# Kernel optimization log

Hardware: AMD Instinct MI355X
Metric: run time of the kernel (lower is better)

The kernel has to match this reference:

```python
import jax, jax.numpy as jnp
import numpy as np

N = 50000      # num nodes
E = 800000     # num edges
IN = 512       # in_feats (= num_hidden)
H = 8          # num_heads
D = 64         # out_feats per head (H*D = 512)
NEG_SLOPE = 0.2


def setup_inputs() -> dict:
    key = jax.random.key(0)
    ks = jax.random.split(key, 7)
    feat = jax.random.normal(ks[0], (N, IN), jnp.float32)
    src = jax.random.randint(ks[1], (E,), 0, N)
    dst = jax.random.randint(ks[2], (E,), 0, N)
    W_fc = jax.random.normal(ks[3], (IN, H * D), jnp.float32) * (1.0 / np.sqrt(IN))
    W_res = jax.random.normal(ks[4], (IN, H * D), jnp.float32) * (1.0 / np.sqrt(IN))
    attn_l = jax.random.normal(ks[5], (1, H, D), jnp.float32) * 0.1
    attn_r = jax.random.normal(ks[6], (1, H, D), jnp.float32) * 0.1
    return {"feat": feat, "src": src, "dst": dst, "W_fc": W_fc,
            "W_res": W_res, "attn_l": attn_l, "attn_r": attn_r}


def reference(feat, src, dst, W_fc, W_res, attn_l, attn_r):
    # fc: [N, IN] @ [IN, H*D] -> [N, H, D]
    ft = (feat @ W_fc).reshape(N, H, D)
    # attention logits per node: el = sum(ft * attn_l, -1), er likewise -> [N, H]
    el = jnp.sum(ft * attn_l, axis=-1)
    er = jnp.sum(ft * attn_r, axis=-1)
    # u_add_v on edges, then LeakyReLU -> [E, H]
    e = jax.nn.leaky_relu(el[src] + er[dst], negative_slope=NEG_SLOPE)
    # edge_softmax: normalize over incoming edges of each dst node
    m = jax.ops.segment_max(e, dst, num_segments=N)            # [N, H]
    m = jnp.where(jnp.isfinite(m), m, jnp.zeros_like(m))       # guard zero-in-degree
    ex = jnp.exp(e - m[dst])                                   # [E, H]
    s = jax.ops.segment_sum(ex, dst, num_segments=N)           # [N, H]
    a = ex / jnp.maximum(s[dst], 1e-9)                         # [E, H]
    # u_mul_e + sum aggregation: gather src features, weight, scatter-add to dst
    msg = ft[src] * a[:, :, None]                              # [E, H, D]
    rst = jax.ops.segment_sum(msg, dst, num_segments=N)        # [N, H, D]
    # residual: res_fc Linear since in_dst_feats != out_feats
    rst = rst + (feat @ W_res).reshape(N, H, D)
    return rst
```

## Files before the change

### kernel.cpp

```cpp
#include <hip/hip_runtime.h>
#include <hip/hip_bf16.h>

#define NN 50000
#define EE 800000
#define INF 512
#define HH 8
#define DD 64
#define HD 512

typedef unsigned short u16;
typedef u16 u16x4 __attribute__((ext_vector_type(4)));
typedef u16 u16x8 __attribute__((ext_vector_type(8)));
typedef __bf16 bf16x8 __attribute__((ext_vector_type(8)));
typedef float f32x4 __attribute__((ext_vector_type(4)));

__device__ __forceinline__ float bf2f(u16 u) {
    return __uint_as_float(((unsigned)u) << 16);
}
__device__ __forceinline__ u16 f2bf(float f) {
    __hip_bfloat16 h = __float2bfloat16(f);
    return *reinterpret_cast<u16*>(&h);
}

__device__ __forceinline__ void gload_lds16(const void* g, void* l) {
    __builtin_amdgcn_global_load_lds(
        (const __attribute__((address_space(1))) void*)g,
        (__attribute__((address_space(3))) void*)l, 16, 0, 0);
}

__global__ __launch_bounds__(256) void sniff5_kernel(const u16* __restrict__ p0,
                                                     const u16* __restrict__ p1,
                                                     const u16* __restrict__ p2,
                                                     const u16* __restrict__ p3,
                                                     const u16* __restrict__ p4,
                                                     int* __restrict__ flags) {
    const u16* ps[5] = {p0, p1, p2, p3, p4};
    const u16* p = ps[blockIdx.x];
    __shared__ int bad;
    if (threadIdx.x == 0) bad = 0;
    __syncthreads();
    float v = fabsf(bf2f(p[2 * threadIdx.x]));
    if (!(v < 1e4f)) atomicAdd(&bad, 1);
    __syncthreads();
    if (threadIdx.x == 0) flags[blockIdx.x] = (bad >= 8) ? 1 : 0;
}

__global__ __launch_bounds__(256) void convert_kernel(const void* __restrict__ in,
                                                      u16* __restrict__ out,
                                                      const int* __restrict__ flag) {
    const int isf32 = *flag;
    const int total = NN * INF / 8;
    for (int i = blockIdx.x * 256 + threadIdx.x; i < total; i += gridDim.x * 256) {
        if (isf32) {
            f32x4 a = ((const f32x4*)in)[2 * i];
            f32x4 b = ((const f32x4*)in)[2 * i + 1];
            u16x8 w;
#pragma unroll
            for (int j = 0; j < 4; ++j) { w[j] = f2bf(a[j]); w[4 + j] = f2bf(b[j]); }
            ((u16x8*)out)[i] = w;
        } else {
            ((u16x8*)out)[i] = ((const u16x8*)in)[i];
        }
    }
}

__global__ __launch_bounds__(256) void transpose_kernel(const void* __restrict__ in,
                                                        u16* __restrict__ out,
                                                        const int* __restrict__ flag) {
    __shared__ u16 tile[64][65];
    const int isf32 = *flag;
    int tr = (blockIdx.x & 7) * 64;
    int tc = (blockIdx.x >> 3) * 64;
    for (int idx = threadIdx.x; idx < 64 * 64; idx += 256) {
        int r = idx >> 6, c = idx & 63;
        int g = (tr + r) * 512 + tc + c;
        tile[r][c] = isf32 ? f2bf(((const float*)in)[g]) : ((const u16*)in)[g];
    }
    __syncthreads();
    for (int idx = threadIdx.x; idx < 64 * 64; idx += 256) {
        int r = idx >> 6, c = idx & 63;
        out[(tc + r) * 512 + tr + c] = tile[c][r];
    }
}

__global__ void zero_deg_kernel(int* __restrict__ deg) {
    int t = blockIdx.x * 256 + threadIdx.x;
    if (t < NN) deg[t] = 0;
}

__global__ void count_kernel(const int* __restrict__ dst, int* __restrict__ deg) {
    int e = blockIdx.x * 256 + threadIdx.x;
    if (e < EE) atomicAdd(&deg[dst[e]], 1);
}

#define SCAN_CH 49
__global__ __launch_bounds__(1024) void scan_kernel(const int* __restrict__ deg,
                                                    int* __restrict__ rowptr,
                                                    int* __restrict__ cursor) {
    __shared__ int sums[1024];
    int t = threadIdx.x;
    int base = t * SCAN_CH;
    int s = 0;
    for (int k = 0; k < SCAN_CH; ++k) {
        int i = base + k;
        if (i < NN) s += deg[i];
    }
    sums[t] = s;
    __syncthreads();
    for (int off = 1; off < 1024; off <<= 1) {
        int v = (t >= off) ? sums[t - off] : 0;
        __syncthreads();
        sums[t] += v;
        __syncthreads();
    }
    int run = (t == 0) ? 0 : sums[t - 1];
    for (int k = 0; k < SCAN_CH; ++k) {
        int i = base + k;
        if (i < NN) {
            rowptr[i] = run;
            cursor[i] = run;
            run += deg[i];
        }
    }
    if (t == 0) rowptr[NN] = EE;
}

__global__ void scatter_kernel(const int* __restrict__ src, const int* __restrict__ dst,
                               int* __restrict__ cursor, int* __restrict__ csr_src) {
    int e = blockIdx.x * 256 + threadIdx.x;
    if (e < EE) {
        int p = atomicAdd(&cursor[dst[e]], 1);
        csr_src[p] = src[e];
    }
}

#define TM 128
#define TN 128
#define BK 64
#define NT (INF / BK)
#define NMBLK 392

__global__ __launch_bounds__(256, 5) void gemm_kernel(const u16* __restrict__ Ab,
                                                      const u16* __restrict__ Wt,
                                                      u16* __restrict__ ft,
                                                      float* __restrict__ outf) {
    __shared__ u16 Asm[TM * BK];
    __shared__ u16 Bsm[TN * BK];

    const int bid = blockIdx.x;
    const int r8 = bid & 7;
    const int q = bid >> 3;
    const int m0 = (((q >> 3) << 3) | r8) * TM;
    const int n0 = (q & 7) * TN;
    const int tid = threadIdx.x;
    const int lane = tid & 63;
    const int wave = tid >> 6;
    const int wr = (wave >> 1) * 64;
    const int wc = (wave & 1) * 64;
    const int lrow = lane & 15;
    const int quad = lane >> 4;

    const int rg = lane >> 3;
    const int ch = lane & 7;
    const int cs = ch ^ rg;

    const u16* asrc[4];
    const u16* bsrc[4];
    u16* adst[4];
    u16* bdst[4];
#pragma unroll
    for (int g = 0; g < 4; ++g) {
        int G = wave * 4 + g;
        int r = G * 8 + rg;
        int gr = m0 + r; gr = gr < NN ? gr : NN - 1;
        asrc[g] = Ab + (size_t)gr * INF + cs * 8;
        bsrc[g] = Wt + (size_t)(n0 + r) * INF + cs * 8;
        adst[g] = Asm + G * 512;
        bdst[g] = Bsm + G * 512;
    }

    f32x4 acc[4][4] = {};

    for (int t = 0; t < NT; ++t) {
        const int k0 = t * BK;
        __syncthreads();
#pragma unroll
        for (int g = 0; g < 4; ++g) {
            gload_lds16(asrc[g] + k0, adst[g]);
            gload_lds16(bsrc[g] + k0, bdst[g]);
        }
        __syncthreads();

#pragma unroll
        for (int ks = 0; ks < 2; ++ks) {
            bf16x8 af[4], bfr[4];
#pragma unroll
            for (int mi = 0; mi < 4; ++mi) {
                int ar = wr + mi * 16 + lrow;
                int sc = (ks * 4 + quad) ^ (ar & 7);
                u16x8 tv = *(const u16x8*)(Asm + ar * 64 + sc * 8);
                af[mi] = *(bf16x8*)&tv;
            }
#pragma unroll
            for (int ni = 0; ni < 4; ++ni) {
                int br = wc + ni * 16 + lrow;
                int sc = (ks * 4 + quad) ^ (br & 7);
                u16x8 tv = *(const u16x8*)(Bsm + br * 64 + sc * 8);
                bfr[ni] = *(bf16x8*)&tv;
            }
#pragma unroll
            for (int mi = 0; mi < 4; ++mi)
#pragma unroll
                for (int ni = 0; ni < 4; ++ni)
                    acc[mi][ni] = __builtin_amdgcn_mfma_f32_16x16x32_bf16(af[mi], bfr[ni],
                                                                          acc[mi][ni], 0, 0, 0);
        }
    }

#pragma unroll
    for (int mi = 0; mi < 4; ++mi) {
        int rb = m0 + wr + mi * 16 + quad * 4;
#pragma unroll
        for (int ni = 0; ni < 4; ++ni) {
            int col = n0 + wc + ni * 16 + lrow;
#pragma unroll
            for (int r = 0; r < 4; ++r) {
                int row = rb + r;
                if (row < NN) {
                    float v = acc[mi][ni][r];
                    if (col < HD) ft[row * HD + col] = f2bf(v);
                    else outf[row * HD + (col - HD)] = v;
                }
            }
        }
    }
}

__global__ __launch_bounds__(256) void attn_dot_kernel(const u16* __restrict__ ft,
                                                       const void* __restrict__ al,
                                                       const void* __restrict__ ar,
                                                       float* __restrict__ el,
                                                       float* __restrict__ er,
                                                       const int* __restrict__ flags) {
    int node = blockIdx.x * 4 + (threadIdx.x >> 6);
    if (node >= NN) return;
    int lane = threadIdx.x & 63;
    int off = lane * 8;

    float wl[8], wr_[8];
    if (flags[3]) {
        f32x4 a0 = *(const f32x4*)((const float*)al + off);
        f32x4 a1 = *(const f32x4*)((const float*)al + off + 4);
#pragma unroll
        for (int j = 0; j < 4; ++j) { wl[j] = a0[j]; wl[4 + j] = a1[j]; }
    } else {
        u16x8 a = *(const u16x8*)((const u16*)al + off);
#pragma unroll
        for (int j = 0; j < 8; ++j) wl[j] = bf2f(a[j]);
    }
    if (flags[4]) {
        f32x4 a0 = *(const f32x4*)((const float*)ar + off);
        f32x4 a1 = *(const f32x4*)((const float*)ar + off + 4);
#pragma unroll
        for (int j = 0; j < 4; ++j) { wr_[j] = a0[j]; wr_[4 + j] = a1[j]; }
    } else {
        u16x8 a = *(const u16x8*)((const u16*)ar + off);
#pragma unroll
        for (int j = 0; j < 8; ++j) wr_[j] = bf2f(a[j]);
    }

    u16x8 f = *(const u16x8*)(ft + node * HD + off);
    float vl = 0.0f, vr = 0.0f;
#pragma unroll
    for (int j = 0; j < 8; ++j) {
        float x = bf2f(f[j]);
        vl += x * wl[j];
        vr += x * wr_[j];
    }
#pragma unroll
    for (int msk = 1; msk < 8; msk <<= 1) {
        vl += __shfl_xor(vl, msk);
        vr += __shfl_xor(vr, msk);
    }
    if ((lane & 7) == 0) {
        el[node * HH + (lane >> 3)] = vl;
        er[node * HH + (lane >> 3)] = vr;
    }
}

__global__ __launch_bounds__(256) void aggregate_kernel(const int* __restrict__ rowptr,
                                                        const int* __restrict__ csr_src,
                                                        const u16* __restrict__ ft,
                                                        const float* __restrict__ el,
                                                        const float* __restrict__ er,
                                                        float* __restrict__ outf) {
    int node = blockIdx.x * 2 + (threadIdx.x >> 7);
    if (node >= NN) return;
    int half = (threadIdx.x >> 6) & 1;
    int lane = threadIdx.x & 63;
    int ebase = half * 256 + lane * 4;
    int head = ebase >> 6;
    int beg = rowptr[node], end = rowptr[node + 1];
    float erd = er[node * HH + head];

    float sden = 0.0f;
    float acc0 = 0.f, acc1 = 0.f, acc2 = 0.f, acc3 = 0.f;

    if (beg < end) {
        const int last = end - 1;
        float elp0, elp1, elp2, elp3;
        u16x4 fp0, fp1, fp2, fp3;
        int sn0, sn1, sn2, sn3;
        {
            int c0 = csr_src[min(beg + 0, last)];
            int c1 = csr_src[min(beg + 1, last)];
            int c2 = csr_src[min(beg + 2, last)];
            int c3 = csr_src[min(beg + 3, last)];
            elp0 = el[c0 * HH + head]; fp0 = *(const u16x4*)(ft + c0 * HD + ebase);
            elp1 = el[c1 * HH + head]; fp1 = *(const u16x4*)(ft + c1 * HD + ebase);
            elp2 = el[c2 * HH + head]; fp2 = *(const u16x4*)(ft + c2 * HD + ebase);
            elp3 = el[c3 * HH + head]; fp3 = *(const u16x4*)(ft + c3 * HD + ebase);
            sn0 = csr_src[min(beg + 4, last)];
            sn1 = csr_src[min(beg + 5, last)];
            sn2 = csr_src[min(beg + 6, last)];
            sn3 = csr_src[min(beg + 7, last)];
        }
        for (int base = beg; base < end; base += 4) {
#define PROC(K)                                                              \
            {                                                                \
                float elv = elp##K;                                          \
                u16x4 f = fp##K;                                             \
                int s = sn##K;                                               \
                elp##K = el[s * HH + head];                                  \
                fp##K = *(const u16x4*)(ft + s * HD + ebase);                \
                sn##K = csr_src[min(base + 8 + K, last)];                    \
                float v = elv + erd;                                         \
                v = v > 0.0f ? v : 0.2f * v;                                 \
                v = fminf(v, 75.0f);                                         \
                float ex = __expf(v);                                        \
                ex = (base + K < end) ? ex : 0.0f;                           \
                sden += ex;                                                  \
                acc0 += bf2f(f[0]) * ex;                                     \
                acc1 += bf2f(f[1]) * ex;                                     \
                acc2 += bf2f(f[2]) * ex;                                     \
                acc3 += bf2f(f[3]) * ex;                                     \
            }
            PROC(0) PROC(1) PROC(2) PROC(3)
#undef PROC
        }
    }

    float inv = 1.0f / fmaxf(sden, 1e-9f);
    float* op = outf + node * HD + ebase;
    f32x4 r = *(const f32x4*)op;
    f32x4 o;
    o[0] = acc0 * inv + r[0];
    o[1] = acc1 * inv + r[1];
    o[2] = acc2 * inv + r[2];
    o[3] = acc3 * inv + r[3];
    *(f32x4*)op = o;
}

extern "C" void kernel_launch(void* const* d_in, const int* in_sizes, int n_in,
                              void* d_out, int out_size, void* d_ws, size_t ws_size,
                              hipStream_t stream) {
    const void* feat   = d_in[0];
    const int*  src    = (const int*)d_in[1];
    const int*  dst    = (const int*)d_in[2];
    const void* W_fc   = d_in[3];
    const void* W_res  = d_in[4];
    const void* attn_l = d_in[5];
    const void* attn_r = d_in[6];
    float* outf = (float*)d_out;

    char* ws = (char*)d_ws;
    int*   flags   = (int*)(ws);
    u16*   Wt      = (u16*)(ws + 256);
    u16*   ft      = (u16*)(ws + 1048832);
    float* el      = (float*)(ws + 52248832);
    float* er      = (float*)(ws + 53848832);
    int*   deg     = (int*)(ws + 55448832);
    int*   rowptr  = (int*)(ws + 55648832);
    int*   cursor  = (int*)(ws + 55848896);
    int*   csr_src = (int*)(ws + 56048896);
    u16*   feat16  = (u16*)(ws + 59248896);

    sniff5_kernel<<<5, 256, 0, stream>>>((const u16*)feat, (const u16*)W_fc,
                                         (const u16*)W_res, (const u16*)attn_l,
                                         (const u16*)attn_r, flags);
    convert_kernel<<<2048, 256, 0, stream>>>(feat, feat16, flags + 0);
    transpose_kernel<<<64, 256, 0, stream>>>(W_fc, Wt, flags + 1);
    transpose_kernel<<<64, 256, 0, stream>>>(W_res, Wt + 512 * 512, flags + 2);

    zero_deg_kernel<<<(NN + 255) / 256, 256, 0, stream>>>(deg);
    count_kernel<<<(EE + 255) / 256, 256, 0, stream>>>(dst, deg);
    scan_kernel<<<1, 1024, 0, stream>>>(deg, rowptr, cursor);
    scatter_kernel<<<(EE + 255) / 256, 256, 0, stream>>>(src, dst, cursor, csr_src);

    gemm_kernel<<<NMBLK * 8, 256, 0, stream>>>(feat16, Wt, ft, outf);

    attn_dot_kernel<<<(NN + 3) / 4, 256, 0, stream>>>(ft, attn_l, attn_r, el, er, flags);
    aggregate_kernel<<<(NN + 1) / 2, 256, 0, stream>>>(rowptr, csr_src, ft, el, er, outf);
}
```

Measured before the change: 670.2 us.

## Precompute per-edge attention weights in a separate kernel before aggregation

Adds an edge_weight_kernel that computes exp(leaky_relu(el[src]+er[dst])) for every CSR edge and head, and stores the results contiguously in CSR order. The aggregation kernel then streams these weights instead of gathering el[src] and computing the exponential inline. This turns one random gather per edge into a sequential read. The cost is an extra kernel launch, a 25.6MB weight buffer written and read back, and a csr_dst array written during scatter. The ew buffer reuses the feat16 workspace region, which is safe only because the GEMM has already consumed feat16 by then.

```diff
diff --git a/kernel.cpp b/kernel.cpp
--- a/kernel.cpp
+++ b/kernel.cpp
@@ -126,11 +126,14 @@
 }
 
 __global__ void scatter_kernel(const int* __restrict__ src, const int* __restrict__ dst,
-                               int* __restrict__ cursor, int* __restrict__ csr_src) {
+                               int* __restrict__ cursor, int* __restrict__ csr_src,
+                               int* __restrict__ csr_dst) {
     int e = blockIdx.x * 256 + threadIdx.x;
     if (e < EE) {
-        int p = atomicAdd(&cursor[dst[e]], 1);
+        int d = dst[e];
+        int p = atomicAdd(&cursor[d], 1);
         csr_src[p] = src[e];
+        csr_dst[p] = d;
     }
 }
 
@@ -288,11 +291,27 @@
     }
 }
 
+__global__ __launch_bounds__(256) void edge_weight_kernel(const int* __restrict__ csr_src,
+                                                          const int* __restrict__ csr_dst,
+                                                          const float* __restrict__ el,
+                                                          const float* __restrict__ er,
+                                                          float* __restrict__ ew) {
+    int t = blockIdx.x * 256 + threadIdx.x;
+    int p = t >> 3;
+    if (p >= EE) return;
+    int h = t & 7;
+    int s = csr_src[p];
+    int d = csr_dst[p];
+    float v = el[s * HH + h] + er[d * HH + h];
+    v = v > 0.0f ? v : 0.2f * v;
+    v = fminf(v, 75.0f);
+    ew[p * HH + h] = __expf(v);
+}
+
 __global__ __launch_bounds__(256) void aggregate_kernel(const int* __restrict__ rowptr,
                                                         const int* __restrict__ csr_src,
+                                                        const float* __restrict__ ew,
                                                         const u16* __restrict__ ft,
-                                                        const float* __restrict__ el,
-                                                        const float* __restrict__ er,
                                                         float* __restrict__ outf) {
     int node = blockIdx.x * 2 + (threadIdx.x >> 7);
     if (node >= NN) return;
@@ -301,14 +320,13 @@
     int ebase = half * 256 + lane * 4;
     int head = ebase >> 6;
     int beg = rowptr[node], end = rowptr[node + 1];
-    float erd = er[node * HH + head];
 
     float sden = 0.0f;
     float acc0 = 0.f, acc1 = 0.f, acc2 = 0.f, acc3 = 0.f;
 
     if (beg < end) {
         const int last = end - 1;
-        float elp0, elp1, elp2, elp3;
+        float wp0, wp1, wp2, wp3;
         u16x4 fp0, fp1, fp2, fp3;
         int sn0, sn1, sn2, sn3;
         {
@@ -316,10 +334,14 @@
             int c1 = csr_src[min(beg + 1, last)];
             int c2 = csr_src[min(beg + 2, last)];
             int c3 = csr_src[min(beg + 3, last)];
-            elp0 = el[c0 * HH + head]; fp0 = *(const u16x4*)(ft + c0 * HD + ebase);
-            elp1 = el[c1 * HH + head]; fp1 = *(const u16x4*)(ft + c1 * HD + ebase);
-            elp2 = el[c2 * HH + head]; fp2 = *(const u16x4*)(ft + c2 * HD + ebase);
-            elp3 = el[c3 * HH + head]; fp3 = *(const u16x4*)(ft + c3 * HD + ebase);
+            wp0 = ew[min(beg + 0, last) * HH + head];
+            wp1 = ew[min(beg + 1, last) * HH + head];
+            wp2 = ew[min(beg + 2, last) * HH + head];
+            wp3 = ew[min(beg + 3, last) * HH + head];
+            fp0 = *(const u16x4*)(ft + c0 * HD + ebase);
+            fp1 = *(const u16x4*)(ft + c1 * HD + ebase);
+            fp2 = *(const u16x4*)(ft + c2 * HD + ebase);
+            fp3 = *(const u16x4*)(ft + c3 * HD + ebase);
             sn0 = csr_src[min(beg + 4, last)];
             sn1 = csr_src[min(beg + 5, last)];
             sn2 = csr_src[min(beg + 6, last)];
@@ -328,22 +350,17 @@
         for (int base = beg; base < end; base += 4) {
 #define PROC(K)                                                              \
             {                                                                \
-                float elv = elp##K;                                          \
+                float w = (base + K < end) ? wp##K : 0.0f;                   \
                 u16x4 f = fp##K;                                             \
                 int s = sn##K;                                               \
-                elp##K = el[s * HH + head];                                  \
+                wp##K = ew[min(base + 4 + K, last) * HH + head];             \
                 fp##K = *(const u16x4*)(ft + s * HD + ebase);                \
                 sn##K = csr_src[min(base + 8 + K, last)];                    \
-                float v = elv + erd;                                         \
-                v = v > 0.0f ? v : 0.2f * v;                                 \
-                v = fminf(v, 75.0f);                                         \
-                float ex = __expf(v);                                        \
-                ex = (base + K < end) ? ex : 0.0f;                           \
-                sden += ex;                                                  \
-                acc0 += bf2f(f[0]) * ex;                                     \
-                acc1 += bf2f(f[1]) * ex;                                     \
-                acc2 += bf2f(f[2]) * ex;                                     \
-                acc3 += bf2f(f[3]) * ex;                                     \
+                sden += w;                                                   \
+                acc0 += bf2f(f[0]) * w;                                      \
+                acc1 += bf2f(f[1]) * w;                                      \
+                acc2 += bf2f(f[2]) * w;                                      \
+                acc3 += bf2f(f[3]) * w;                                      \
             }
             PROC(0) PROC(1) PROC(2) PROC(3)
 #undef PROC
@@ -384,6 +401,8 @@
     int*   cursor  = (int*)(ws + 55848896);
     int*   csr_src = (int*)(ws + 56048896);
     u16*   feat16  = (u16*)(ws + 59248896);
+    float* ew      = (float*)(ws + 59248896);
+    int*   csr_dst = (int*)(ws + 110448896);
 
     sniff5_kernel<<<5, 256, 0, stream>>>((const u16*)feat, (const u16*)W_fc,
                                          (const u16*)W_res, (const u16*)attn_l,
@@ -395,10 +414,11 @@
     zero_deg_kernel<<<(NN + 255) / 256, 256, 0, stream>>>(deg);
     count_kernel<<<(EE + 255) / 256, 256, 0, stream>>>(dst, deg);
     scan_kernel<<<1, 1024, 0, stream>>>(deg, rowptr, cursor);
-    scatter_kernel<<<(EE + 255) / 256, 256, 0, stream>>>(src, dst, cursor, csr_src);
+    scatter_kernel<<<(EE + 255) / 256, 256, 0, stream>>>(src, dst, cursor, csr_src, csr_dst);
 
     gemm_kernel<<<NMBLK * 8, 256, 0, stream>>>(feat16, Wt, ft, outf);
 
     attn_dot_kernel<<<(NN + 3) / 4, 256, 0, stream>>>(ft, attn_l, attn_r, el, er, flags);
-    aggregate_kernel<<<(NN + 1) / 2, 256, 0, stream>>>(rowptr, csr_src, ft, el, er, outf);
-}
+    edge_weight_kernel<<<EE * 8 / 256, 256, 0, stream>>>(csr_src, csr_dst, el, er, ew);
+    aggregate_kernel<<<(NN + 1) / 2, 256, 0, stream>>>(rowptr, csr_src, ew, ft, outf);
+}
```

After: 690.1 us. 1.03x slower.

## Fuse prep kernels into one launch and compute attention dots in GEMM epilogue

Applied to the files above, without the earlier changes.

Merges the dtype sniff, feature conversion, weight transposes and degree zeroing into a single prep kernel in which each block sniffs its own input. The el/er attention dot products are now computed from the fp32 GEMM accumulators in the epilogue, using shuffles across the 16 lanes, so the separate attn_dot pass that re-read ft is gone. This saves several launches and one full read of the bf16 ft array. In exchange every conversion block repeats the sniff, and the GEMM epilogue gains extra shuffles and possible register pressure. el/er also now come from fp32 accumulators rather than rounded bf16, which changes numerics slightly.

```diff
diff --git a/kernel.cpp b/kernel.cpp
--- a/kernel.cpp
+++ b/kernel.cpp
@@ -28,64 +28,68 @@
         (__attribute__((address_space(3))) void*)l, 16, 0, 0);
 }
 
-__global__ __launch_bounds__(256) void sniff5_kernel(const u16* __restrict__ p0,
-                                                     const u16* __restrict__ p1,
-                                                     const u16* __restrict__ p2,
-                                                     const u16* __restrict__ p3,
-                                                     const u16* __restrict__ p4,
-                                                     int* __restrict__ flags) {
-    const u16* ps[5] = {p0, p1, p2, p3, p4};
-    const u16* p = ps[blockIdx.x];
-    __shared__ int bad;
-    if (threadIdx.x == 0) bad = 0;
+__device__ __forceinline__ int sniff_region(const u16* __restrict__ p, int* vote) {
+    int tid = threadIdx.x;
+    if (tid == 0) *vote = 0;
     __syncthreads();
-    float v = fabsf(bf2f(p[2 * threadIdx.x]));
-    if (!(v < 1e4f)) atomicAdd(&bad, 1);
+    float v = fabsf(bf2f(p[2 * tid]));
+    if (!(v < 1e4f)) atomicAdd(vote, 1);
     __syncthreads();
-    if (threadIdx.x == 0) flags[blockIdx.x] = (bad >= 8) ? 1 : 0;
-}
-
-__global__ __launch_bounds__(256) void convert_kernel(const void* __restrict__ in,
-                                                      u16* __restrict__ out,
-                                                      const int* __restrict__ flag) {
-    const int isf32 = *flag;
-    const int total = NN * INF / 8;
-    for (int i = blockIdx.x * 256 + threadIdx.x; i < total; i += gridDim.x * 256) {
-        if (isf32) {
-            f32x4 a = ((const f32x4*)in)[2 * i];
-            f32x4 b = ((const f32x4*)in)[2 * i + 1];
-            u16x8 w;
-#pragma unroll
-            for (int j = 0; j < 4; ++j) { w[j] = f2bf(a[j]); w[4 + j] = f2bf(b[j]); }
-            ((u16x8*)out)[i] = w;
-        } else {
-            ((u16x8*)out)[i] = ((const u16x8*)in)[i];
-        }
-    }
-}
-
-__global__ __launch_bounds__(256) void transpose_kernel(const void* __restrict__ in,
-                                                        u16* __restrict__ out,
-                                                        const int* __restrict__ flag) {
+    int r = (*vote >= 8) ? 1 : 0;
+    __syncthreads();
+    return r;
+}
+
+#define PREP_CONV 2048
+#define PREP_TR   (PREP_CONV + 128)
+#define PREP_ZERO (PREP_TR + 196)
+
+__global__ __launch_bounds__(256) void prep_kernel(const void* __restrict__ feat,
+                                                   u16* __restrict__ feat16,
+                                                   const void* __restrict__ W_fc,
+                                                   const void* __restrict__ W_res,
+                                                   u16* __restrict__ Wt,
+                                                   int* __restrict__ deg) {
     __shared__ u16 tile[64][65];
-    const int isf32 = *flag;
-    int tr = (blockIdx.x & 7) * 64;
-    int tc = (blockIdx.x >> 3) * 64;
-    for (int idx = threadIdx.x; idx < 64 * 64; idx += 256) {
-        int r = idx >> 6, c = idx & 63;
-        int g = (tr + r) * 512 + tc + c;
-        tile[r][c] = isf32 ? f2bf(((const float*)in)[g]) : ((const u16*)in)[g];
-    }
-    __syncthreads();
-    for (int idx = threadIdx.x; idx < 64 * 64; idx += 256) {
-        int r = idx >> 6, c = idx & 63;
-        out[(tc + r) * 512 + tr + c] = tile[c][r];
-    }
-}
-
-__global__ void zero_deg_kernel(int* __restrict__ deg) {
-    int t = blockIdx.x * 256 + threadIdx.x;
-    if (t < NN) deg[t] = 0;
+    const int bid = blockIdx.x;
+    const int tid = threadIdx.x;
+    if (bid < PREP_CONV) {
+        const int isf32 = sniff_region((const u16*)feat, (int*)&tile[0][0]);
+        const int total = NN * INF / 8;
+        for (int i = bid * 256 + tid; i < total; i += PREP_CONV * 256) {
+            if (isf32) {
+                f32x4 a = ((const f32x4*)feat)[2 * i];
+                f32x4 b = ((const f32x4*)feat)[2 * i + 1];
+                u16x8 w;
+#pragma unroll
+                for (int j = 0; j < 4; ++j) { w[j] = f2bf(a[j]); w[4 + j] = f2bf(b[j]); }
+                ((u16x8*)feat16)[i] = w;
+            } else {
+                ((u16x8*)feat16)[i] = ((const u16x8*)feat)[i];
+            }
+        }
+    } else if (bid < PREP_TR) {
+        const int w = bid - PREP_CONV;
+        const void* in = (w < 64) ? W_fc : W_res;
+        u16* out = Wt + ((w < 64) ? 0 : 512 * 512);
+        const int tb = w & 63;
+        const int isf32 = sniff_region((const u16*)in, (int*)&tile[0][0]);
+        int tr = (tb & 7) * 64;
+        int tc = (tb >> 3) * 64;
+        for (int idx = tid; idx < 64 * 64; idx += 256) {
+            int r = idx >> 6, c = idx & 63;
+            int g = (tr + r) * 512 + tc + c;
+            tile[r][c] = isf32 ? f2bf(((const float*)in)[g]) : ((const u16*)in)[g];
+        }
+        __syncthreads();
+        for (int idx = tid; idx < 64 * 64; idx += 256) {
+            int r = idx >> 6, c = idx & 63;
+            out[(tc + r) * 512 + tr + c] = tile[c][r];
+        }
+    } else {
+        int t = (bid - PREP_TR) * 256 + tid;
+        if (t < NN) deg[t] = 0;
+    }
 }
 
 __global__ void count_kernel(const int* __restrict__ dst, int* __restrict__ deg) {
@@ -143,7 +147,11 @@
 __global__ __launch_bounds__(256, 5) void gemm_kernel(const u16* __restrict__ Ab,
                                                       const u16* __restrict__ Wt,
                                                       u16* __restrict__ ft,
-                                                      float* __restrict__ outf) {
+                                                      float* __restrict__ outf,
+                                                      const void* __restrict__ al,
+                                                      const void* __restrict__ ar,
+                                                      float* __restrict__ el,
+                                                      float* __restrict__ er) {
     __shared__ u16 Asm[TM * BK];
     __shared__ u16 Bsm[TN * BK];
 
@@ -196,9 +204,9 @@
             bf16x8 af[4], bfr[4];
 #pragma unroll
             for (int mi = 0; mi < 4; ++mi) {
-                int ar = wr + mi * 16 + lrow;
-                int sc = (ks * 4 + quad) ^ (ar & 7);
-                u16x8 tv = *(const u16x8*)(Asm + ar * 64 + sc * 8);
+                int ar_ = wr + mi * 16 + lrow;
+                int sc = (ks * 4 + quad) ^ (ar_ & 7);
+                u16x8 tv = *(const u16x8*)(Asm + ar_ * 64 + sc * 8);
                 af[mi] = *(bf16x8*)&tv;
             }
 #pragma unroll
@@ -234,57 +242,41 @@
             }
         }
     }
-}
-
-__global__ __launch_bounds__(256) void attn_dot_kernel(const u16* __restrict__ ft,
-                                                       const void* __restrict__ al,
-                                                       const void* __restrict__ ar,
-                                                       float* __restrict__ el,
-                                                       float* __restrict__ er,
-                                                       const int* __restrict__ flags) {
-    int node = blockIdx.x * 4 + (threadIdx.x >> 6);
-    if (node >= NN) return;
-    int lane = threadIdx.x & 63;
-    int off = lane * 8;
-
-    float wl[8], wr_[8];
-    if (flags[3]) {
-        f32x4 a0 = *(const f32x4*)((const float*)al + off);
-        f32x4 a1 = *(const f32x4*)((const float*)al + off + 4);
-#pragma unroll
-        for (int j = 0; j < 4; ++j) { wl[j] = a0[j]; wl[4 + j] = a1[j]; }
-    } else {
-        u16x8 a = *(const u16x8*)((const u16*)al + off);
-#pragma unroll
-        for (int j = 0; j < 8; ++j) wl[j] = bf2f(a[j]);
-    }
-    if (flags[4]) {
-        f32x4 a0 = *(const f32x4*)((const float*)ar + off);
-        f32x4 a1 = *(const f32x4*)((const float*)ar + off + 4);
-#pragma unroll
-        for (int j = 0; j < 4; ++j) { wr_[j] = a0[j]; wr_[4 + j] = a1[j]; }
-    } else {
-        u16x8 a = *(const u16x8*)((const u16*)ar + off);
-#pragma unroll
-        for (int j = 0; j < 8; ++j) wr_[j] = bf2f(a[j]);
-    }
-
-    u16x8 f = *(const u16x8*)(ft + node * HD + off);
-    float vl = 0.0f, vr = 0.0f;
-#pragma unroll
-    for (int j = 0; j < 8; ++j) {
-        float x = bf2f(f[j]);
-        vl += x * wl[j];
-        vr += x * wr_[j];
-    }
-#pragma unroll
-    for (int msk = 1; msk < 8; msk <<= 1) {
-        vl += __shfl_xor(vl, msk);
-        vr += __shfl_xor(vr, msk);
-    }
-    if ((lane & 7) == 0) {
-        el[node * HH + (lane >> 3)] = vl;
-        er[node * HH + (lane >> 3)] = vr;
+
+    if (n0 < HD) {
+        __syncthreads();
+        const int fal = sniff_region((const u16*)al, (int*)Asm);
+        const int far_ = sniff_region((const u16*)ar, (int*)Asm);
+        const int h = (n0 >> 6) + (wc >> 6);
+        float alv[4], arv[4];
+#pragma unroll
+        for (int ni = 0; ni < 4; ++ni) {
+            int idx = h * DD + ni * 16 + lrow;
+            alv[ni] = fal ? ((const float*)al)[idx] : bf2f(((const u16*)al)[idx]);
+            arv[ni] = far_ ? ((const float*)ar)[idx] : bf2f(((const u16*)ar)[idx]);
+        }
+#pragma unroll
+        for (int mi = 0; mi < 4; ++mi) {
+#pragma unroll
+            for (int r = 0; r < 4; ++r) {
+                float se = 0.0f, sr = 0.0f;
+#pragma unroll
+                for (int ni = 0; ni < 4; ++ni) {
+                    se += acc[mi][ni][r] * alv[ni];
+                    sr += acc[mi][ni][r] * arv[ni];
+                }
+#pragma unroll
+                for (int m = 1; m < 16; m <<= 1) {
+                    se += __shfl_xor(se, m);
+                    sr += __shfl_xor(sr, m);
+                }
+                int row = m0 + wr + mi * 16 + quad * 4 + r;
+                if (lrow == 0 && row < NN) {
+                    el[row * HH + h] = se;
+                    er[row * HH + h] = sr;
+                }
+            }
+        }
     }
 }
 
@@ -374,7 +366,6 @@
     float* outf = (float*)d_out;
 
     char* ws = (char*)d_ws;
-    int*   flags   = (int*)(ws);
     u16*   Wt      = (u16*)(ws + 256);
     u16*   ft      = (u16*)(ws + 1048832);
     float* el      = (float*)(ws + 52248832);
@@ -385,20 +376,13 @@
     int*   csr_src = (int*)(ws + 56048896);
     u16*   feat16  = (u16*)(ws + 59248896);
 
-    sniff5_kernel<<<5, 256, 0, stream>>>((const u16*)feat, (const u16*)W_fc,
-                                         (const u16*)W_res, (const u16*)attn_l,
-                                         (const u16*)attn_r, flags);
-    convert_kernel<<<2048, 256, 0, stream>>>(feat, feat16, flags + 0);
-    transpose_kernel<<<64, 256, 0, stream>>>(W_fc, Wt, flags + 1);
-    transpose_kernel<<<64, 256, 0, stream>>>(W_res, Wt + 512 * 512, flags + 2);
-
-    zero_deg_kernel<<<(NN + 255) / 256, 256, 0, stream>>>(deg);
+    prep_kernel<<<PREP_ZERO, 256, 0, stream>>>(feat, feat16, W_fc, W_res, Wt, deg);
     count_kernel<<<(EE + 255) / 256, 256, 0, stream>>>(dst, deg);
     scan_kernel<<<1, 1024, 0, stream>>>(deg, rowptr, cursor);
     scatter_kernel<<<(EE + 255) / 256, 256, 0, stream>>>(src, dst, cursor, csr_src);
 
-    gemm_kernel<<<NMBLK * 8, 256, 0, stream>>>(feat16, Wt, ft, outf);
-
-    attn_dot_kernel<<<(NN + 3) / 4, 256, 0, stream>>>(ft, attn_l, attn_r, el, er, flags);
+    gemm_kernel<<<NMBLK * 8, 256, 0, stream>>>(feat16, Wt, ft, outf,
+                                               attn_l, attn_r, el, er);
+
     aggregate_kernel<<<(NN + 1) / 2, 256, 0, stream>>>(rowptr, csr_src, ft, el, er, outf);
 }
```

Result: slower. 715.1 us (+6.7%).
